# Optimization experiments

Measured on AMD Instinct MI355X. Metric: run time of the kernel, lower is better.

## Reference

```python
import jax, jax.numpy as jnp
import numpy as np

NEG_INF = -1e10
SLOPE = 0.01  # LeakyReLU default negative slope

def _lrelu(x):
    return jnp.where(x >= 0, x, SLOPE * x)

def setup_inputs() -> dict:
    key = jax.random.key(0)
    ks = jax.random.split(key, 12)
    B, L, D = 64, 512, 512
    s = 1.0 / np.sqrt(D)
    s2 = 1.0 / np.sqrt(2 * D)
    return {
        "r1": jax.random.normal(ks[0], (B, L, D), jnp.float32),
        "r2": jax.random.normal(ks[1], (B, L, D), jnp.float32),
        "mask1": jax.random.randint(ks[2], (B, L, 1), 0, 2, jnp.int32),
        "mask2": jax.random.randint(ks[3], (B, L, 1), 0, 2, jnp.int32),
        # mlp params (shared for r1 and r2, as in the torch module)
        "W1": jax.random.uniform(ks[4], (D, D), jnp.float32, -s, s),
        "b1": jnp.zeros((D,), jnp.float32),
        "W2": jax.random.uniform(ks[5], (D, D), jnp.float32, -s, s),
        "b2": jnp.zeros((D,), jnp.float32),
        # compare params
        "Wc1": jax.random.uniform(ks[6], (2 * D, D), jnp.float32, -s2, s2),
        "bc1": jnp.zeros((D,), jnp.float32),
        "Wc2": jax.random.uniform(ks[7], (D, D), jnp.float32, -s, s),
        "bc2": jnp.zeros((D,), jnp.float32),
    }

def reference(r1, r2, mask1, mask2, W1, b1, W2, b2, Wc1, bc1, Wc2, bc2):
    # dropout is inference-mode identity
    def mlp(x):
        return _lrelu(_lrelu(x @ W1 + b1) @ W2 + b2)

    def compare(x):
        return _lrelu(_lrelu(x @ Wc1 + bc1) @ Wc2 + bc2)

    m1 = mask1.astype(jnp.float32)  # [B,L1,1]
    m2 = mask2.astype(jnp.float32)  # [B,L2,1]
    r1m = mlp(r1) * m1
    r2m = mlp(r2) * m2

    # pairwise mask: >0 iff both tokens valid (magnitude from the D-dim matmul is irrelevant)
    mpos = m1 * jnp.swapaxes(m2, 1, 2)            # [B,L1,L2] in {0,1}
    mask_inf = jnp.where(mpos > 0, 0.0, NEG_INF)  # additive mask

    o = jnp.einsum('bik,bjk->bij', r1m, r2m) + mask_inf  # [B,L1,L2]
    o1 = jax.nn.softmax(o, axis=2) * mpos
    o2 = jax.nn.softmax(o, axis=1) * mpos

    r1_c = jnp.einsum('bij,bjd->bid', o1, r2m)  # [B,L1,D]
    r2_c = jnp.einsum('bij,bid->bjd', o2, r1m)  # [B,L2,D]

    r1_cmp = compare(jnp.concatenate([r1m, r1_c], axis=-1)) * m1
    r2_cmp = compare(jnp.concatenate([r2m, r2_c], axis=-1)) * m2
    return (r1_cmp, r2_cmp)
```

## Files before the change

kernel.cpp:

```cpp
#include <hip/hip_runtime.h>

#define LRELU_SLOPE 0.01f
#define NEG_BIG -1e10f

typedef unsigned short ushort_t;
typedef __bf16 bf16x8 __attribute__((ext_vector_type(8)));
typedef float f32x4 __attribute__((ext_vector_type(4)));

static __device__ __forceinline__ float lrelu_f(float x) {
    return x >= 0.0f ? x : LRELU_SLOPE * x;
}

static __device__ __forceinline__ ushort_t f2bf(float f) {
    unsigned int u = __float_as_uint(f);
    u += 0x7fffu + ((u >> 16) & 1u);
    return (ushort_t)(u >> 16);
}

static __device__ __forceinline__ void gld_lds16(const ushort_t* g, ushort_t* l) {
    __builtin_amdgcn_global_load_lds((const __attribute__((address_space(1))) void*)g,
                                     (__attribute__((address_space(3))) void*)l,
                                     16, 0, 0);
}

template<bool BIAS, bool LRELU, bool RM, bool PM, bool BF16OUT, bool TWOUT>
__global__ __launch_bounds__(512, 2)
void gemm_nt(const ushort_t* __restrict__ A0, const ushort_t* __restrict__ A1,
             int Ksplit, int lda0, int lda1,
             const ushort_t* __restrict__ B, int ldb,
             const float* __restrict__ bias,
             const int* __restrict__ rm1, const int* __restrict__ rm2,
             void* __restrict__ C, int ldc,
             ushort_t* __restrict__ CT, int Mhalf,
             int M, int N, int K,
             long sA, long sB, long sC)
{
    __shared__ ushort_t lds[2][2][256 * 64];

    const unsigned nbx = gridDim.x, nby = gridDim.y;
    unsigned lin = blockIdx.x + nbx * (blockIdx.y + nby * blockIdx.z);
    const unsigned nwg = nbx * nby * gridDim.z;
    if ((nwg & 7u) == 0u)
        lin = (lin & 7u) * (nwg >> 3) + (lin >> 3);
    const unsigned bxs = lin % nbx;
    const unsigned t1  = lin / nbx;
    const unsigned bys = t1 % nby;
    const unsigned bzs = t1 / nby;

    const int bz   = (int)bzs;
    const int tid  = threadIdx.x;
    const int w    = tid >> 6;
    const int lane = tid & 63;
    const int wm   = w >> 2;
    const int wn   = w & 3;
    const int row0 = (int)bys * 256;
    const int col0 = (int)bxs * 256;

    const ushort_t* Ab0 = A0 + (long)bz * sA;
    const ushort_t* Ab1 = A1 + (long)bz * sA;
    const ushort_t* Bb  = B  + (long)bz * sB;

    const int sr = w * 32 + (lane >> 3);
    const int so = (((lane & 7) ^ ((lane >> 3) & 7)) * 8);

    const int lr = lane & 15, q = lane >> 4;
    const int cx0 = ((q ^ (lr & 7)) * 8);
    const int cx1 = (((q + 4) ^ (lr & 7)) * 8);
    const int aRow = (wm * 128 + lr) * 64;
    const int bRow = (wn * 64 + lr) * 64;

    f32x4 acc[8][4] = {};

    auto stage = [&](int T, int buf) {
        const int k0g = T << 6;
        const ushort_t* Ap; int kk0, ldaP;
        if (k0g < Ksplit) { Ap = Ab0; kk0 = k0g;          ldaP = lda0; }
        else              { Ap = Ab1; kk0 = k0g - Ksplit; ldaP = lda1; }
        ushort_t* Ad = &lds[buf][0][0];
        ushort_t* Bd = &lds[buf][1][0];
        #pragma unroll
        for (int u = 0; u < 4; ++u)
            gld_lds16(Ap + (size_t)(row0 + sr + u * 8) * ldaP + kk0 + so,
                      Ad + (w * 32 + u * 8) * 64);
        #pragma unroll
        for (int u = 0; u < 4; ++u)
            gld_lds16(Bb + (size_t)(col0 + sr + u * 8) * ldb + k0g + so,
                      Bd + (w * 32 + u * 8) * 64);
    };

    const int NT = K >> 6;
    stage(0, 0);

    for (int T = 0; T < NT; ++T) {
        const int buf = T & 1;
        asm volatile("s_waitcnt vmcnt(0)" ::: "memory");
        __builtin_amdgcn_s_barrier();
        if (T + 1 < NT) stage(T + 1, buf ^ 1);

        const ushort_t* Abuf = &lds[buf][0][0];
        const ushort_t* Bbuf = &lds[buf][1][0];

        bf16x8 af[4][2], bf[2][2];
        #pragma unroll
        for (int p = 0; p < 4; ++p) {
            const int mh = p >> 1, nh = p & 1;
            if (nh == 0) {
                #pragma unroll
                for (int ii = 0; ii < 4; ++ii) {
                    const int rb = aRow + (mh * 64 + ii * 16) * 64;
                    af[ii][0] = *reinterpret_cast<const bf16x8*>(&Abuf[rb + cx0]);
                    af[ii][1] = *reinterpret_cast<const bf16x8*>(&Abuf[rb + cx1]);
                }
            }
            #pragma unroll
            for (int jj = 0; jj < 2; ++jj) {
                const int rb = bRow + (nh * 32 + jj * 16) * 64;
                bf[jj][0] = *reinterpret_cast<const bf16x8*>(&Bbuf[rb + cx0]);
                bf[jj][1] = *reinterpret_cast<const bf16x8*>(&Bbuf[rb + cx1]);
            }
            asm volatile("s_waitcnt lgkmcnt(0)" ::: "memory");
            __builtin_amdgcn_sched_barrier(0);
            __builtin_amdgcn_s_setprio(1);
            #pragma unroll
            for (int ii = 0; ii < 4; ++ii)
                #pragma unroll
                for (int jj = 0; jj < 2; ++jj)
                    #pragma unroll
                    for (int kk = 0; kk < 2; ++kk)
                        acc[mh * 4 + ii][nh * 2 + jj] =
                            __builtin_amdgcn_mfma_f32_16x16x32_bf16(
                                af[ii][kk], bf[jj][kk],
                                acc[mh * 4 + ii][nh * 2 + jj], 0, 0, 0);
            __builtin_amdgcn_s_setprio(0);
            if (p < 3) __builtin_amdgcn_s_barrier();
        }
    }

    float biasv[4];
    int mj[4];
    #pragma unroll
    for (int j = 0; j < 4; ++j) {
        const int c = col0 + wn * 64 + j * 16 + lr;
        if (BIAS) biasv[j] = bias[c];
        if (PM)   mj[j] = rm2[(long)bz * N + c];
    }
    float* Cf = (float*)C + (long)bz * sC;
    ushort_t* Ch = (ushort_t*)C + (long)bz * sC;

    #pragma unroll
    for (int i = 0; i < 8; ++i) {
        const int rg0 = row0 + wm * 128 + i * 16 + q * 4;
        int mi4[4];
        if (RM || PM) {
            #pragma unroll
            for (int r = 0; r < 4; ++r) {
                const int row = rg0 + r;
                if (PM)      mi4[r] = rm1[(long)bz * M + row];
                else         mi4[r] = (row < Mhalf) ? rm1[row] : rm2[row - Mhalf];
            }
        }
        #pragma unroll
        for (int j = 0; j < 4; ++j) {
            const int c = col0 + wn * 64 + j * 16 + lr;
            ushort_t tp[4];
            #pragma unroll
            for (int r = 0; r < 4; ++r) {
                const int row = rg0 + r;
                float v = acc[i][j][r];
                if (BIAS) v += biasv[j];
                if (LRELU) v = lrelu_f(v);
                if (RM) v *= (float)mi4[r];
                if (PM) { if (!(mi4[r] && mj[j])) v += NEG_BIG; }
                const size_t a = (size_t)row * ldc + c;
                if (BF16OUT) Ch[a] = f2bf(v); else Cf[a] = v;
                if (TWOUT) tp[r] = f2bf(v);
            }
            if (TWOUT) {
                const size_t ta = ((size_t)(((rg0 >> 9) + 64) & 127)) * 262144
                                + (size_t)c * 512 + (rg0 & 511);
                *reinterpret_cast<uint2*>(CT + ta) = *reinterpret_cast<uint2*>(tp);
            }
        }
    }
}

__global__ __launch_bounds__(256)
void cvt2_f32_bf16(const float* __restrict__ a, const float* __restrict__ b,
                   ushort_t* __restrict__ oa, ushort_t* __restrict__ ob)
{
    const float* in = blockIdx.y ? b : a;
    ushort_t* out = blockIdx.y ? ob : oa;
    const long i = ((long)blockIdx.x * 256 + threadIdx.x) * 4;
    const float4 v = *reinterpret_cast<const float4*>(in + i);
    ushort_t o[4] = { f2bf(v.x), f2bf(v.y), f2bf(v.z), f2bf(v.w) };
    *reinterpret_cast<uint2*>(out + i) = *reinterpret_cast<uint2*>(o);
}

__global__ __launch_bounds__(256)
void transpose_cvt4(const float* __restrict__ W1, const float* __restrict__ W2,
                    const float* __restrict__ Wc1, const float* __restrict__ Wc2,
                    ushort_t* __restrict__ W1t, ushort_t* __restrict__ W2t,
                    ushort_t* __restrict__ Wc1t, ushort_t* __restrict__ Wc2t)
{
    __shared__ float t[32][33];
    const int z = blockIdx.z;
    const float* in = (z == 0) ? W1 : (z == 1) ? W2 : (z == 2) ? Wc1 : Wc2;
    ushort_t* out   = (z == 0) ? W1t : (z == 1) ? W2t : (z == 2) ? Wc1t : Wc2t;
    const int R = (z == 2) ? 1024 : 512;
    const int C = 512;
    const int c0 = blockIdx.x * 32, r0 = blockIdx.y * 32;
    if (r0 >= R) return;
    const int tx = threadIdx.x & 31, ty = threadIdx.x >> 5;
    #pragma unroll
    for (int p = 0; p < 4; ++p)
        t[ty + p * 8][tx] = in[(size_t)(r0 + ty + p * 8) * C + c0 + tx];
    __syncthreads();
    #pragma unroll
    for (int p = 0; p < 4; ++p)
        out[(size_t)(c0 + ty + p * 8) * R + r0 + tx] = f2bf(t[tx][ty + p * 8]);
}

__global__ __launch_bounds__(256)
void row_stats(const float* __restrict__ o, float* __restrict__ rmax,
               float* __restrict__ rsinv, int L)
{
    const int row  = blockIdx.x * 4 + (threadIdx.x >> 6);
    const int lane = threadIdx.x & 63;
    const float* p = o + (long)row * L;
    float m = -3.0e38f;
    for (int j = lane; j < L; j += 64) m = fmaxf(m, p[j]);
    #pragma unroll
    for (int off = 32; off > 0; off >>= 1) m = fmaxf(m, __shfl_xor(m, off));
    float s = 0.0f;
    for (int j = lane; j < L; j += 64) s += __expf(p[j] - m);
    #pragma unroll
    for (int off = 32; off > 0; off >>= 1) s += __shfl_xor(s, off);
    if (lane == 0) { rmax[row] = m; rsinv[row] = 1.0f / s; }
}

__global__ __launch_bounds__(256)
void col_part(const float* __restrict__ o, float* __restrict__ pm,
              float* __restrict__ ps, int L)
{
    const int b  = blockIdx.z;
    const int rc = blockIdx.y;
    const int j  = blockIdx.x * 256 + threadIdx.x;
    const float* p = o + (long)b * L * L + (long)rc * 64 * L + j;
    float m = -3.0e38f, s = 0.0f;
    #pragma unroll 4
    for (int i = 0; i < 64; ++i) {
        const float x = p[(long)i * L];
        const float mn = fmaxf(m, x);
        s = s * __expf(m - mn) + __expf(x - mn);
        m = mn;
    }
    const long idx = ((long)b * 8 + rc) * L + j;
    pm[idx] = m;
    ps[idx] = s;
}

__global__ __launch_bounds__(256)
void col_combine(const float* __restrict__ pm, const float* __restrict__ ps,
                 float* __restrict__ cmax, float* __restrict__ csinv, int L)
{
    const int b = blockIdx.y;
    const int j = blockIdx.x * 256 + threadIdx.x;
    float mk[8], sk[8];
    #pragma unroll
    for (int k = 0; k < 8; ++k) {
        mk[k] = pm[((long)b * 8 + k) * L + j];
        sk[k] = ps[((long)b * 8 + k) * L + j];
    }
    float m = -3.0e38f;
    #pragma unroll
    for (int k = 0; k < 8; ++k) m = fmaxf(m, mk[k]);
    float s = 0.0f;
    #pragma unroll
    for (int k = 0; k < 8; ++k) s += sk[k] * __expf(mk[k] - m);
    cmax[b * L + j]  = m;
    csinv[b * L + j] = 1.0f / s;
}

__global__ __launch_bounds__(256)
void softmax_apply(const float* __restrict__ o,
                   ushort_t* __restrict__ o1, ushort_t* __restrict__ o2T,
                   const float* __restrict__ rmax, const float* __restrict__ rsinv,
                   const float* __restrict__ cmax, const float* __restrict__ csinv,
                   const int* __restrict__ m1, const int* __restrict__ m2)
{
    __shared__ ushort_t t[32][33];
    const int b = blockIdx.z;
    const long bo = (long)b * 512 * 512;
    const int j0 = blockIdx.x * 32, i0 = blockIdx.y * 32;
    const int tx = threadIdx.x & 31, ty = threadIdx.x >> 5;
    const int col = b * 512 + j0 + tx;
    const int mjv = m2[col];
    const float cm = cmax[col], cs = csinv[col];
    #pragma unroll
    for (int p = 0; p < 4; ++p) {
        const int i = i0 + ty + p * 8;
        const int row = b * 512 + i;
        const float x = o[bo + (long)i * 512 + j0 + tx];
        const float mp = (m1[row] != 0 && mjv != 0) ? 1.0f : 0.0f;
        o1[bo + (long)i * 512 + j0 + tx] = f2bf(__expf(x - rmax[row]) * rsinv[row] * mp);
        t[ty + p * 8][tx] = f2bf(__expf(x - cm) * cs * mp);
    }
    __syncthreads();
    #pragma unroll
    for (int p = 0; p < 4; ++p)
        o2T[bo + (long)(j0 + ty + p * 8) * 512 + i0 + tx] = t[tx][ty + p * 8];
}

extern "C" void kernel_launch(void* const* d_in, const int* in_sizes, int n_in,
                              void* d_out, int out_size, void* d_ws, size_t ws_size,
                              hipStream_t stream)
{
    const float* r1  = (const float*)d_in[0];
    const float* r2  = (const float*)d_in[1];
    const int*   m1  = (const int*)d_in[2];
    const int*   m2  = (const int*)d_in[3];
    const float* W1  = (const float*)d_in[4];
    const float* b1v = (const float*)d_in[5];
    const float* W2  = (const float*)d_in[6];
    const float* b2v = (const float*)d_in[7];
    const float* Wc1 = (const float*)d_in[8];
    const float* bc1 = (const float*)d_in[9];
    const float* Wc2 = (const float*)d_in[10];
    const float* bc2 = (const float*)d_in[11];
    float* out = (float*)d_out;

    constexpr int  Bn = 64, L = 512, D = 512;
    constexpr long CE = (long)Bn * L * D;
    constexpr long S  = (long)L * L;
    constexpr int  NR = Bn * L;

    ushort_t* O    = (ushort_t*)d_out;
    ushort_t* r1b  = O;
    ushort_t* r2b  = O + CE;
    ushort_t* TT   = O;
    ushort_t* o1b  = O + 2 * CE;
    ushort_t* o2Tb = O + 3 * CE;

    char* wsb = (char*)d_ws;
    ushort_t* hb   = (ushort_t*)wsb;
    float*    obuf = (float*)wsb;
    ushort_t* r1c  = (ushort_t*)wsb;
    ushort_t* hc   = (ushort_t*)(wsb + 4 * CE);
    ushort_t* r1mb = (ushort_t*)(wsb + 8 * CE);
    ushort_t* r2mb = (ushort_t*)(wsb + 10 * CE);
    ushort_t* W1t  = (ushort_t*)(wsb + 12 * CE);
    ushort_t* W2t  = W1t + 512 * 512;
    ushort_t* Wc1t = W2t + 512 * 512;
    ushort_t* Wc2t = Wc1t + 512 * 1024;
    float* rmaxv = (float*)(Wc2t + 512 * 512);
    float* rsinv = rmaxv + NR;
    float* cmaxv = rsinv + NR;
    float* csinv = cmaxv + NR;
    float* pmbuf = csinv + NR;
    float* psbuf = pmbuf + 8 * L * Bn;

    const dim3 blk(256);
    const dim3 blkG(512);
    const dim3 gD2(D / 256, 2 * NR / 256, 1);
    const dim3 gB(L / 256, L / 256, Bn);
    const dim3 gB2(L / 256, L / 256, 2 * Bn);

    cvt2_f32_bf16<<<dim3(CE / 1024, 2), blk, 0, stream>>>(r1, r2, r1b, r2b);
    transpose_cvt4<<<dim3(16, 32, 4), blk, 0, stream>>>(
        W1, W2, Wc1, Wc2, W1t, W2t, Wc1t, Wc2t);

    gemm_nt<true,true,false,false,true,false><<<gD2, blkG, 0, stream>>>(
        r1b, r1b, D, D, D, W1t, D, b1v, nullptr, nullptr, hb, D,
        nullptr, 0, 2 * NR, D, D, 0, 0, 0);
    gemm_nt<true,true,true,false,true,true><<<gD2, blkG, 0, stream>>>(
        hb, hb, D, D, D, W2t, D, b2v, m1, m2, r1mb, D,
        TT, NR, 2 * NR, D, D, 0, 0, 0);
    gemm_nt<false,false,false,true,false,false><<<gB, blkG, 0, stream>>>(
        r1mb, r1mb, D, D, D, r2mb, D, nullptr, m1, m2, obuf, L,
        nullptr, 0, L, L, D, S, S, S);
    row_stats<<<dim3(NR / 4), blk, 0, stream>>>(obuf, rmaxv, rsinv, L);
    col_part<<<dim3(L / 256, 8, Bn), blk, 0, stream>>>(obuf, pmbuf, psbuf, L);
    col_combine<<<dim3(L / 256, Bn), blk, 0, stream>>>(pmbuf, psbuf, cmaxv, csinv, L);
    softmax_apply<<<dim3(16, 16, Bn), blk, 0, stream>>>(
        obuf, o1b, o2Tb, rmaxv, rsinv, cmaxv, csinv, m1, m2);
    gemm_nt<false,false,false,false,true,false><<<gB2, blkG, 0, stream>>>(
        o1b, o1b, L, L, L, TT, L, nullptr, nullptr, nullptr, r1c, D,
        nullptr, 0, L, D, L, S, S, S);
    gemm_nt<true,true,false,false,true,false><<<gD2, blkG, 0, stream>>>(
        r1mb, r1c, D, D, D, Wc1t, 2 * D, bc1, nullptr, nullptr, hc, D,
        nullptr, 0, 2 * NR, D, 2 * D, 0, 0, 0);
    gemm_nt<true,true,true,false,false,false><<<gD2, blkG, 0, stream>>>(
        hc, hc, D, D, D, Wc2t, D, bc2, m1, m2, out, D,
        nullptr, NR, 2 * NR, D, D, 0, 0, 0);
}
```

Before: 610.1 us.

## Split tile loads into partial waits so compute starts before full A tile arrives

Reorders the global-to-LDS staging so B and the first half of A rows (for mh=0) are issued first, then the second half of A. The main loop now waits with vmcnt(2) before the first half of compute and vmcnt(8) before the second half, instead of waiting for everything. It also cuts the per-quarter barriers from three to one mid-tile barrier. The goal is to overlap the tail of each global load with MFMA work and reduce synchronisation. The tradeoff is fragile vmcnt accounting that depends on the exact order in which loads are issued.

```diff
diff --git a/kernel.cpp b/kernel.cpp
--- a/kernel.cpp
+++ b/kernel.cpp
@@ -60,8 +60,8 @@
     const ushort_t* Ab1 = A1 + (long)bz * sA;
     const ushort_t* Bb  = B  + (long)bz * sB;
 
-    const int sr = w * 32 + (lane >> 3);
-    const int so = (((lane & 7) ^ ((lane >> 3) & 7)) * 8);
+    const int srr = w * 8 + (lane >> 3);
+    const int so  = (((lane & 7) ^ ((lane >> 3) & 7)) * 8);
 
     const int lr = lane & 15, q = lane >> 4;
     const int cx0 = ((q ^ (lr & 7)) * 8);
@@ -80,12 +80,17 @@
         ushort_t* Bd = &lds[buf][1][0];
         #pragma unroll
         for (int u = 0; u < 4; ++u)
-            gld_lds16(Ap + (size_t)(row0 + sr + u * 8) * ldaP + kk0 + so,
-                      Ad + (w * 32 + u * 8) * 64);
-        #pragma unroll
-        for (int u = 0; u < 4; ++u)
-            gld_lds16(Bb + (size_t)(col0 + sr + u * 8) * ldb + k0g + so,
-                      Bd + (w * 32 + u * 8) * 64);
+            gld_lds16(Bb + (size_t)(col0 + u * 64 + srr) * ldb + k0g + so,
+                      Bd + (u * 64 + w * 8) * 64);
+        gld_lds16(Ap + (size_t)(row0 + 0 * 64 + srr) * ldaP + kk0 + so,
+                  Ad + (0 * 64 + w * 8) * 64);
+        gld_lds16(Ap + (size_t)(row0 + 2 * 64 + srr) * ldaP + kk0 + so,
+                  Ad + (2 * 64 + w * 8) * 64);
+        __builtin_amdgcn_sched_barrier(0);
+        gld_lds16(Ap + (size_t)(row0 + 1 * 64 + srr) * ldaP + kk0 + so,
+                  Ad + (1 * 64 + w * 8) * 64);
+        gld_lds16(Ap + (size_t)(row0 + 3 * 64 + srr) * ldaP + kk0 + so,
+                  Ad + (3 * 64 + w * 8) * 64);
     };
 
     const int NT = K >> 6;
@@ -93,46 +98,54 @@
 
     for (int T = 0; T < NT; ++T) {
         const int buf = T & 1;
-        asm volatile("s_waitcnt vmcnt(0)" ::: "memory");
-        __builtin_amdgcn_s_barrier();
-        if (T + 1 < NT) stage(T + 1, buf ^ 1);
-
         const ushort_t* Abuf = &lds[buf][0][0];
         const ushort_t* Bbuf = &lds[buf][1][0];
 
-        bf16x8 af[4][2], bf[2][2];
+        asm volatile("s_waitcnt vmcnt(2)" ::: "memory");
+        __builtin_amdgcn_s_barrier();
+        asm volatile("" ::: "memory");
+        if (T + 1 < NT) stage(T + 1, buf ^ 1);
+
         #pragma unroll
-        for (int p = 0; p < 4; ++p) {
-            const int mh = p >> 1, nh = p & 1;
-            if (nh == 0) {
+        for (int mh = 0; mh < 2; ++mh) {
+            if (mh == 1) {
+                if (T + 1 < NT)
+                    asm volatile("s_waitcnt vmcnt(8)" ::: "memory");
+                else
+                    asm volatile("s_waitcnt vmcnt(0)" ::: "memory");
+                __builtin_amdgcn_s_barrier();
+                asm volatile("" ::: "memory");
+            }
+            bf16x8 af[4][2], bf[2][2];
+            #pragma unroll
+            for (int ii = 0; ii < 4; ++ii) {
+                const int rb = aRow + (mh * 64 + ii * 16) * 64;
+                af[ii][0] = *reinterpret_cast<const bf16x8*>(&Abuf[rb + cx0]);
+                af[ii][1] = *reinterpret_cast<const bf16x8*>(&Abuf[rb + cx1]);
+            }
+            #pragma unroll
+            for (int nh = 0; nh < 2; ++nh) {
                 #pragma unroll
-                for (int ii = 0; ii < 4; ++ii) {
-                    const int rb = aRow + (mh * 64 + ii * 16) * 64;
-                    af[ii][0] = *reinterpret_cast<const bf16x8*>(&Abuf[rb + cx0]);
-                    af[ii][1] = *reinterpret_cast<const bf16x8*>(&Abuf[rb + cx1]);
+                for (int jj = 0; jj < 2; ++jj) {
+                    const int rb = bRow + (nh * 32 + jj * 16) * 64;
+                    bf[jj][0] = *reinterpret_cast<const bf16x8*>(&Bbuf[rb + cx0]);
+                    bf[jj][1] = *reinterpret_cast<const bf16x8*>(&Bbuf[rb + cx1]);
                 }
-            }
-            #pragma unroll
-            for (int jj = 0; jj < 2; ++jj) {
-                const int rb = bRow + (nh * 32 + jj * 16) * 64;
-                bf[jj][0] = *reinterpret_cast<const bf16x8*>(&Bbuf[rb + cx0]);
-                bf[jj][1] = *reinterpret_cast<const bf16x8*>(&Bbuf[rb + cx1]);
-            }
-            asm volatile("s_waitcnt lgkmcnt(0)" ::: "memory");
-            __builtin_amdgcn_sched_barrier(0);
-            __builtin_amdgcn_s_setprio(1);
-            #pragma unroll
-            for (int ii = 0; ii < 4; ++ii)
+                asm volatile("s_waitcnt lgkmcnt(0)" ::: "memory");
+                __builtin_amdgcn_sched_barrier(0);
+                __builtin_amdgcn_s_setprio(1);
                 #pragma unroll
-                for (int jj = 0; jj < 2; ++jj)
+                for (int ii = 0; ii < 4; ++ii)
                     #pragma unroll
-                    for (int kk = 0; kk < 2; ++kk)
-                        acc[mh * 4 + ii][nh * 2 + jj] =
-                            __builtin_amdgcn_mfma_f32_16x16x32_bf16(
-                                af[ii][kk], bf[jj][kk],
-                                acc[mh * 4 + ii][nh * 2 + jj], 0, 0, 0);
-            __builtin_amdgcn_s_setprio(0);
-            if (p < 3) __builtin_amdgcn_s_barrier();
+                    for (int jj = 0; jj < 2; ++jj)
+                        #pragma unroll
+                        for (int kk = 0; kk < 2; ++kk)
+                            acc[mh * 4 + ii][nh * 2 + jj] =
+                                __builtin_amdgcn_mfma_f32_16x16x32_bf16(
+                                    af[ii][kk], bf[jj][kk],
+                                    acc[mh * 4 + ii][nh * 2 + jj], 0, 0, 0);
+                __builtin_amdgcn_s_setprio(0);
+            }
         }
     }
 
```

Result: no change. 600.8 us (-1.5%).

## Use 1024-thread GEMM blocks with 16 waves and split barriers

Applied to the files above, without the earlier changes.

The 256x256-tile bf16 GEMM now runs with 16 waves (1024 threads) instead of 8, so each wave owns a 64x64 sub-tile with half the accumulators and issues half as many global-to-LDS loads. The K loop no longer needs a barrier between each quarter-tile step. The prefetch of the next tile is now issued before waiting on the current one (vmcnt(4)), letting loads overlap. This is meant to raise latency hiding through more waves and fewer intra-loop barriers, at the cost of more per-block synchronisation and possible register pressure under the new launch bounds (1024, 4).

```diff
diff --git a/kernel.cpp b/kernel.cpp
--- a/kernel.cpp
+++ b/kernel.cpp
@@ -24,7 +24,7 @@
 }
 
 template<bool BIAS, bool LRELU, bool RM, bool PM, bool BF16OUT, bool TWOUT>
-__global__ __launch_bounds__(512, 2)
+__global__ __launch_bounds__(1024, 4)
 void gemm_nt(const ushort_t* __restrict__ A0, const ushort_t* __restrict__ A1,
              int Ksplit, int lda0, int lda1,
              const ushort_t* __restrict__ B, int ldb,
@@ -60,16 +60,16 @@
     const ushort_t* Ab1 = A1 + (long)bz * sA;
     const ushort_t* Bb  = B  + (long)bz * sB;
 
-    const int sr = w * 32 + (lane >> 3);
-    const int so = (((lane & 7) ^ ((lane >> 3) & 7)) * 8);
+    const int srr = w * 16 + (lane >> 3);
+    const int so  = (((lane & 7) ^ ((lane >> 3) & 7)) * 8);
 
     const int lr = lane & 15, q = lane >> 4;
     const int cx0 = ((q ^ (lr & 7)) * 8);
     const int cx1 = (((q + 4) ^ (lr & 7)) * 8);
-    const int aRow = (wm * 128 + lr) * 64;
+    const int aRow = (wm * 64 + lr) * 64;
     const int bRow = (wn * 64 + lr) * 64;
 
-    f32x4 acc[8][4] = {};
+    f32x4 acc[4][4] = {};
 
     auto stage = [&](int T, int buf) {
         const int k0g = T << 6;
@@ -79,13 +79,13 @@
         ushort_t* Ad = &lds[buf][0][0];
         ushort_t* Bd = &lds[buf][1][0];
         #pragma unroll
-        for (int u = 0; u < 4; ++u)
-            gld_lds16(Ap + (size_t)(row0 + sr + u * 8) * ldaP + kk0 + so,
-                      Ad + (w * 32 + u * 8) * 64);
+        for (int u = 0; u < 2; ++u)
+            gld_lds16(Ap + (size_t)(row0 + srr + u * 8) * ldaP + kk0 + so,
+                      Ad + (w * 16 + u * 8) * 64);
         #pragma unroll
-        for (int u = 0; u < 4; ++u)
-            gld_lds16(Bb + (size_t)(col0 + sr + u * 8) * ldb + k0g + so,
-                      Bd + (w * 32 + u * 8) * 64);
+        for (int u = 0; u < 2; ++u)
+            gld_lds16(Bb + (size_t)(col0 + srr + u * 8) * ldb + k0g + so,
+                      Bd + (w * 16 + u * 8) * 64);
     };
 
     const int NT = K >> 6;
@@ -93,46 +93,40 @@
 
     for (int T = 0; T < NT; ++T) {
         const int buf = T & 1;
-        asm volatile("s_waitcnt vmcnt(0)" ::: "memory");
-        __builtin_amdgcn_s_barrier();
-        if (T + 1 < NT) stage(T + 1, buf ^ 1);
-
         const ushort_t* Abuf = &lds[buf][0][0];
         const ushort_t* Bbuf = &lds[buf][1][0];
 
-        bf16x8 af[4][2], bf[2][2];
+        __builtin_amdgcn_s_barrier();
+        asm volatile("" ::: "memory");
+        if (T + 1 < NT) {
+            stage(T + 1, buf ^ 1);
+            asm volatile("s_waitcnt vmcnt(4)" ::: "memory");
+        } else {
+            asm volatile("s_waitcnt vmcnt(0)" ::: "memory");
+        }
+        __builtin_amdgcn_s_barrier();
+        asm volatile("" ::: "memory");
+
         #pragma unroll
-        for (int p = 0; p < 4; ++p) {
-            const int mh = p >> 1, nh = p & 1;
-            if (nh == 0) {
-                #pragma unroll
-                for (int ii = 0; ii < 4; ++ii) {
-                    const int rb = aRow + (mh * 64 + ii * 16) * 64;
-                    af[ii][0] = *reinterpret_cast<const bf16x8*>(&Abuf[rb + cx0]);
-                    af[ii][1] = *reinterpret_cast<const bf16x8*>(&Abuf[rb + cx1]);
-                }
-            }
-            #pragma unroll
-            for (int jj = 0; jj < 2; ++jj) {
-                const int rb = bRow + (nh * 32 + jj * 16) * 64;
-                bf[jj][0] = *reinterpret_cast<const bf16x8*>(&Bbuf[rb + cx0]);
-                bf[jj][1] = *reinterpret_cast<const bf16x8*>(&Bbuf[rb + cx1]);
-            }
+        for (int kk = 0; kk < 2; ++kk) {
+            const int cx = kk ? cx1 : cx0;
+            bf16x8 af[4], bf[4];
+            #pragma unroll
+            for (int ii = 0; ii < 4; ++ii)
+                af[ii] = *reinterpret_cast<const bf16x8*>(&Abuf[aRow + (ii * 16) * 64 + cx]);
+            #pragma unroll
+            for (int jj = 0; jj < 4; ++jj)
+                bf[jj] = *reinterpret_cast<const bf16x8*>(&Bbuf[bRow + (jj * 16) * 64 + cx]);
             asm volatile("s_waitcnt lgkmcnt(0)" ::: "memory");
             __builtin_amdgcn_sched_barrier(0);
             __builtin_amdgcn_s_setprio(1);
             #pragma unroll
             for (int ii = 0; ii < 4; ++ii)
                 #pragma unroll
-                for (int jj = 0; jj < 2; ++jj)
-                    #pragma unroll
-                    for (int kk = 0; kk < 2; ++kk)
-                        acc[mh * 4 + ii][nh * 2 + jj] =
-                            __builtin_amdgcn_mfma_f32_16x16x32_bf16(
-                                af[ii][kk], bf[jj][kk],
-                                acc[mh * 4 + ii][nh * 2 + jj], 0, 0, 0);
+                for (int jj = 0; jj < 4; ++jj)
+                    acc[ii][jj] = __builtin_amdgcn_mfma_f32_16x16x32_bf16(
+                        af[ii], bf[jj], acc[ii][jj], 0, 0, 0);
             __builtin_amdgcn_s_setprio(0);
-            if (p < 3) __builtin_amdgcn_s_barrier();
         }
     }
 
@@ -148,8 +142,8 @@
     ushort_t* Ch = (ushort_t*)C + (long)bz * sC;
 
     #pragma unroll
-    for (int i = 0; i < 8; ++i) {
-        const int rg0 = row0 + wm * 128 + i * 16 + q * 4;
+    for (int i = 0; i < 4; ++i) {
+        const int rg0 = row0 + wm * 64 + i * 16 + q * 4;
         int mi4[4];
         if (RM || PM) {
             #pragma unroll
@@ -360,7 +354,7 @@
     float* psbuf = pmbuf + 8 * L * Bn;
 
     const dim3 blk(256);
-    const dim3 blkG(512);
+    const dim3 blkG(1024);
     const dim3 gD2(D / 256, 2 * NR / 256, 1);
     const dim3 gB(L / 256, L / 256, Bn);
     const dim3 gB2(L / 256, L / 256, 2 * Bn);
```

New measurement: 609.4 us. About the same (-0.1%).
